# Kernel optimization log

Hardware: AMD Instinct MI355X
Metric: run time of the kernel (lower is better)

Reference implementation:

```python
import jax, jax.numpy as jnp
import numpy as np

B, F_IN, N, S = 2, 128, 192, 192   # batch, in_features, n_nodes, seq (seq==n_nodes required by mask broadcast)
H, D = 4, 64                        # n_heads, n_hidden (out_features = H*D = 256)
NEG_SLOPE = 0.2


def setup_inputs() -> dict:
    key = jax.random.key(0)
    ks = jax.random.split(key, 6)
    X = jax.random.normal(ks[0], (B, F_IN, N, S), dtype=jnp.float32)
    A = jax.random.randint(ks[1], (N, N, 1), 0, 2, dtype=jnp.int32)
    W_lin = jax.random.normal(ks[2], (F_IN, H * D), dtype=jnp.float32) * 0.05
    b_lin = jax.random.uniform(ks[3], (H * D,), dtype=jnp.float32)
    W_attn = jax.random.normal(ks[4], (2 * D,), dtype=jnp.float32) * 0.05
    b_attn = jax.random.uniform(ks[5], (1,), dtype=jnp.float32)
    return {"X": X, "A": A, "W_lin": W_lin, "b_lin": b_lin,
            "W_attn": W_attn, "b_attn": b_attn}


def reference(X, A, W_lin, b_lin, W_attn, b_attn):
    # Dropout is identity (eval mode).
    b, f, n, s = X.shape
    x = jnp.transpose(X, (0, 3, 2, 1))                      # (b, s, n, f)
    g = (x @ W_lin + b_lin).reshape(b, s, n, H, D)          # (b, s, n, H, D)
    # attn is affine: attn(cat[g_i, g_j]) = a_src.g_i + a_dst.g_j + b_attn
    a_src, a_dst = W_attn[:D], W_attn[D:]
    s_src = jnp.einsum('bsnhd,d->bsnh', g, a_src)
    s_dst = jnp.einsum('bsnhd,d->bsnh', g, a_dst)
    e = s_src[:, :, :, None, :] + s_dst[:, :, None, :, :] + b_attn[0]  # (b, s, n_i, n_j, H)
    e = jnp.where(e >= 0, e, NEG_SLOPE * e)                 # LeakyReLU
    # torch masked_fill broadcast: mask (n,n,1,1) aligns with e dims (s, n_i, n_j, H)
    e = jnp.where(A[..., None] == 0, -jnp.inf, e)
    alphas = jax.nn.softmax(e, axis=1)                      # softmax over seq dim (dim=1, as in source)
    alphas = jnp.nan_to_num(alphas, nan=0.0)
    # einsum 'mnojh,klphf->mnohf': independent sums over j (alphas) and k,l,p (g)
    sum_g = g.sum(axis=(0, 1, 2))                           # (H, D)
    attn_res = alphas.sum(axis=3)[..., None] * sum_g        # (b, s, n, H, D)
    out = attn_res.reshape(b, s, n, H * D)                  # concat=True
    return jnp.transpose(out, (0, 3, 2, 1))                 # (b, out_features, n, s)
```

## Files before the change

kernel.cpp:

```cpp
#include <hip/hip_runtime.h>
#include <math.h>

#define B_ 2
#define F_ 128
#define N_ 192
#define S_ 192
#define NS_ (N_ * S_)
#define SLOPE 0.2f
#define LOG2E 1.4426950408889634f
#define NEG_INF (-__builtin_inff())

#if defined(__has_builtin)
#if __has_builtin(__builtin_amdgcn_exp2f)
#define EXP2(x) __builtin_amdgcn_exp2f(x)
#else
#define EXP2(x) exp2f(x)
#endif
#else
#define EXP2(x) exp2f(x)
#endif

#define OFF_WSRC 0
#define OFF_WDST 512
#define OFF_CSRC 1024
#define OFF_CDST 1028
#define OFF_SUMG 1040
#define OFF_PART 1296
#define OFF_PE   2320
#define OFF_QD   (OFF_PE + 8 * NS_ * 2)
#define OFF_QT   (OFF_QD + 8 * NS_)

__global__ __launch_bounds__(256) void kPre(const float* __restrict__ X,
                                            const float* __restrict__ W_lin,
                                            const float* __restrict__ b_lin,
                                            const float* __restrict__ W_attn,
                                            const float* __restrict__ b_attn,
                                            float* __restrict__ ws) {
    int blk = blockIdx.x, t = threadIdx.x;
    if (blk < 1024) {
        int sq = blk & 3, f = (blk >> 2) & 127, b = blk >> 9;
        const float4* p = (const float4*)(X + ((size_t)(b * F_ + f)) * NS_ + sq * 9216);
        float acc = 0.f;
#pragma unroll
        for (int k = 0; k < 9; k++) {
            float4 v = p[t + k * 256];
            acc += (v.x + v.y) + (v.z + v.w);
        }
        for (int o = 32; o; o >>= 1) acc += __shfl_down(acc, o, 64);
        __shared__ float red[4];
        if ((t & 63) == 0) red[t >> 6] = acc;
        __syncthreads();
        if (t == 0)
            ws[OFF_PART + sq * 256 + b * 128 + f] = (red[0] + red[1]) + (red[2] + red[3]);
    } else if (blk == 1024) {
        const float4* wa = (const float4*)W_attn;
        for (int c = t; c < 512; c += 256) {
            int f = c >> 2, h = c & 3;
            const float4* wl = (const float4*)(W_lin + f * 256 + h * 64);
            float as = 0.f, ad = 0.f;
#pragma unroll
            for (int q = 0; q < 16; q++) {
                float4 w = wl[q], a1 = wa[q], a2 = wa[16 + q];
                as += w.x * a1.x + w.y * a1.y + w.z * a1.z + w.w * a1.w;
                ad += w.x * a2.x + w.y * a2.y + w.z * a2.z + w.w * a2.w;
            }
            ws[OFF_WSRC + c] = as * LOG2E;
            ws[OFF_WDST + c] = ad * LOG2E;
        }
    } else {
        if (t < 4) {
            float c = 0.f;
            for (int d = 0; d < 64; d++) c += b_lin[t * 64 + d] * W_attn[d];
            ws[OFF_CSRC + t] = (c + b_attn[0]) * LOG2E;
        } else if (t < 8) {
            int h = t - 4;
            float c = 0.f;
            for (int d = 0; d < 64; d++) c += b_lin[h * 64 + d] * W_attn[64 + d];
            ws[OFF_CDST + h] = c * LOG2E;
        }
    }
}

__global__ __launch_bounds__(256) void kProj(const float* __restrict__ X,
                                             const int* __restrict__ A,
                                             const float* __restrict__ W_lin,
                                             const float* __restrict__ b_lin,
                                             float* __restrict__ ws) {
    __shared__ float4 wsl[128], wdl[128];
    __shared__ float red[4 * 64 * 9];
    __shared__ float xs[128];
    __shared__ float wbuf[4096];
    int t = threadIdx.x, blk = blockIdx.x;
    if (blk < 1152) {
        int n = blk % 192, bsc = blk / 192;
        int b = bsc / 3, sc = bsc % 3;
        if (t < 128) {
            wsl[t] = ((const float4*)(ws + OFF_WSRC))[t];
            wdl[t] = ((const float4*)(ws + OFF_WDST))[t];
        }
        __syncthreads();
        int fq = t >> 6, lane = t & 63;
        int s = sc * 64 + lane;
        float aS[4] = {0, 0, 0, 0}, aD[4] = {0, 0, 0, 0};
        const float* xp = X + (size_t)(b * F_) * NS_ + n * S_ + s;
        int f0 = fq * 32;
#pragma unroll 8
        for (int fi = 0; fi < 32; fi++) {
            float x = xp[(size_t)(f0 + fi) * NS_];
            float4 w1 = wsl[f0 + fi], w2 = wdl[f0 + fi];
            aS[0] += x * w1.x; aS[1] += x * w1.y; aS[2] += x * w1.z; aS[3] += x * w1.w;
            aD[0] += x * w2.x; aD[1] += x * w2.y; aD[2] += x * w2.z; aD[3] += x * w2.w;
        }
        float* rp = red + t * 9;
#pragma unroll
        for (int h = 0; h < 4; h++) { rp[h] = aS[h]; rp[4 + h] = aD[h]; }
        __syncthreads();
        float2* PEp = (float2*)(ws + OFF_PE);
        float*  QDf = ws + OFF_QD;
        float*  QTf = ws + OFF_QT;
#pragma unroll
        for (int c = t; c < 512; c += 256) {
            int s_loc = c >> 3, k = c & 7;
            float v = red[s_loc * 9 + k] + red[(64 + s_loc) * 9 + k] +
                      red[(128 + s_loc) * 9 + k] + red[(192 + s_loc) * 9 + k];
            int ss = sc * 64 + s_loc;
            if (k < 4) {
                int bh = b * 4 + k;
                bool masked = (A[ss * 192 + n] == 0);
                float2 pr;
                if (masked) { pr.x = 0.f; pr.y = 0.f; }
                else {
                    float pt = v + ws[OFF_CSRC + k];
                    pr.x = EXP2(pt); pr.y = EXP2(0.2f * pt);
                }
                PEp[(size_t)bh * NS_ + n * 192 + ss] = pr;
            } else {
                int h = k - 4, bh = b * 4 + h;
                float dv = v + ws[OFF_CDST + h];
                QDf[(size_t)bh * NS_ + ss * 192 + n] = dv;
                QTf[(size_t)bh * NS_ + n * 192 + ss] = dv;
            }
        }
    } else {
        if (t < 128) {
            float v = 0.f;
#pragma unroll
            for (int q = 0; q < 8; q++) v += ws[OFF_PART + q * 128 + t];
            xs[t] = v;
        }
        float acc = 0.f;
        for (int ch = 0; ch < 8; ch++) {
            const float4* s4 = (const float4*)(W_lin + ch * 4096);
            __syncthreads();
#pragma unroll
            for (int k = 0; k < 4; k++) ((float4*)wbuf)[t + k * 256] = s4[t + k * 256];
            __syncthreads();
#pragma unroll
            for (int fi = 0; fi < 16; fi++) acc += xs[ch * 16 + fi] * wbuf[fi * 256 + t];
        }
        ws[OFF_SUMG + t] = acc + 73728.f * b_lin[t];
    }
}

__global__ __launch_bounds__(576) void kAttn(const float* __restrict__ ws,
                                             float* __restrict__ out) {
    int blk = blockIdx.x, t = threadIdx.x;
    int bh = blk & 7, it = blk >> 3;
    int b = bh >> 2, h = bh & 3;
    __shared__ float4 peA[192];
    __shared__ float2 peB[192];
    __shared__ float zpart[3 * 3 * 192];
    __shared__ float4 zr4[192];
    __shared__ float accp[3 * 3 * 192];
    __shared__ float sg_sh[64];
    const float2* PEp = (const float2*)(ws + OFF_PE) + (size_t)bh * NS_;
    const float*  QDf = ws + OFF_QD + (size_t)bh * NS_;
    const float*  QTf = ws + OFF_QT + (size_t)bh * NS_;
    if (t < 64) sg_sh[t] = ws[OFF_SUMG + h * 64 + t];
    if (t < 192) {
        float2 e0 = PEp[(it * 3 + 0) * 192 + t];
        float2 e1 = PEp[(it * 3 + 1) * 192 + t];
        float2 e2 = PEp[(it * 3 + 2) * 192 + t];
        peA[t] = make_float4(e0.x, e0.y, e1.x, e1.y);
        peB[t] = e2;
    }
    __syncthreads();

    {
        int sq = t / 192, j = t - sq * 192;
        float z0 = 0.f, z1 = 0.f, z2 = 0.f;
#pragma unroll 8
        for (int s = sq * 64; s < sq * 64 + 64; s++) {
            float q = QDf[s * 192 + j];
            float Q1 = EXP2(q), Q2 = EXP2(0.2f * q);
            float4 Ea = peA[s];
            float2 Eb = peB[s];
            z0 += fmaxf(Ea.x * Q1, Ea.y * Q2);
            z1 += fmaxf(Ea.z * Q1, Ea.w * Q2);
            z2 += fmaxf(Eb.x * Q1, Eb.y * Q2);
        }
        zpart[sq * 576 + 0 * 192 + j] = z0;
        zpart[sq * 576 + 1 * 192 + j] = z1;
        zpart[sq * 576 + 2 * 192 + j] = z2;
    }
    __syncthreads();
    {
        int r = t / 192, j = t - r * 192;
        float Z = zpart[r * 192 + j] + zpart[576 + r * 192 + j] +
                  zpart[1152 + r * 192 + j];
        ((float*)zr4)[j * 4 + r] = (Z != 0.f) ? (1.f / Z) : 0.f;
    }
    __syncthreads();

    {
        int jt = t / 192, s = t - jt * 192;
        float4 Ea = peA[s];
        float2 Eb = peB[s];
        float a0 = 0.f, a1 = 0.f, a2 = 0.f;
#pragma unroll 8
        for (int j = jt * 64; j < jt * 64 + 64; j++) {
            float g = QTf[j * 192 + s];
            float G1 = EXP2(g), G2 = EXP2(0.2f * g);
            float4 Z4 = zr4[j];
            a0 += fmaxf(Ea.x * G1, Ea.y * G2) * Z4.x;
            a1 += fmaxf(Ea.z * G1, Ea.w * G2) * Z4.y;
            a2 += fmaxf(Eb.x * G1, Eb.y * G2) * Z4.z;
        }
        accp[jt * 576 + 0 * 192 + s] = a0;
        accp[jt * 576 + 1 * 192 + s] = a1;
        accp[jt * 576 + 2 * 192 + s] = a2;
    }
    __syncthreads();

    {
        int r = t / 192, s = t - r * 192;
        float acc = accp[r * 192 + s] + accp[576 + r * 192 + s] +
                    accp[1152 + r * 192 + s];
        int i = it * 3 + r;
        float* op = out + (((size_t)(b * 256 + h * 64)) * 192 + i) * 192 + s;
#pragma unroll 8
        for (int d = 0; d < 64; d++)
            op[(size_t)d * NS_] = acc * sg_sh[d];
    }
}

extern "C" void kernel_launch(void* const* d_in, const int* in_sizes, int n_in,
                              void* d_out, int out_size, void* d_ws, size_t ws_size,
                              hipStream_t stream) {
    const float* X      = (const float*)d_in[0];
    const int*   A      = (const int*)d_in[1];
    const float* W_lin  = (const float*)d_in[2];
    const float* b_lin  = (const float*)d_in[3];
    const float* W_attn = (const float*)d_in[4];
    const float* b_attn = (const float*)d_in[5];
    float* out = (float*)d_out;
    float* ws  = (float*)d_ws;

    kPre<<<1026, 256, 0, stream>>>(X, W_lin, b_lin, W_attn, b_attn, ws);
    kProj<<<1153, 256, 0, stream>>>(X, A, W_lin, b_lin, ws);
    kAttn<<<512, 576, 0, stream>>>(ws, out);
}
```

Baseline: 163.9 us.

## Fuse three kernels into one persistent kernel with atomic work queues

Replaces the three separate launches (pre-reduction, projection, attention) with a single persistent kernel of 512 blocks. Blocks pull work items from global atomic counters and move between phases through grid-wide completion barriers that spin-wait. The attention phase now writes per-(b,h) accumulators to workspace, and a third phase scales them by sum_g with vectorized float4 stores. This removes launch gaps and tail effects between kernels, but adds spin-wait barriers, an extra workspace round-trip for the accumulators, and depends on all 512 blocks being co-resident.

Result: slower. 310.5 us (+89.5%).

```diff
diff --git a/kernel.cpp b/kernel.cpp
--- a/kernel.cpp
+++ b/kernel.cpp
@@ -6,9 +6,12 @@
 #define N_ 192
 #define S_ 192
 #define NS_ (N_ * S_)
-#define SLOPE 0.2f
 #define LOG2E 1.4426950408889634f
-#define NEG_INF (-__builtin_inff())
+#define NBLK 512
+#define NTHR 384
+#define TOTAL_A 640
+#define TOTAL_B 512
+#define TOTAL_C 512
 
 #if defined(__has_builtin)
 #if __has_builtin(__builtin_amdgcn_exp2f)
@@ -20,227 +23,246 @@
 #define EXP2(x) exp2f(x)
 #endif
 
-#define OFF_WSRC 0
-#define OFF_WDST 512
-#define OFF_CSRC 1024
-#define OFF_CDST 1028
-#define OFF_SUMG 1040
-#define OFF_PART 1296
-#define OFF_PE   2320
+#define OFF_PART 0
+#define OFF_PE   256
 #define OFF_QD   (OFF_PE + 8 * NS_ * 2)
 #define OFF_QT   (OFF_QD + 8 * NS_)
-
-__global__ __launch_bounds__(256) void kPre(const float* __restrict__ X,
-                                            const float* __restrict__ W_lin,
-                                            const float* __restrict__ b_lin,
-                                            const float* __restrict__ W_attn,
-                                            const float* __restrict__ b_attn,
-                                            float* __restrict__ ws) {
-    int blk = blockIdx.x, t = threadIdx.x;
-    if (blk < 1024) {
-        int sq = blk & 3, f = (blk >> 2) & 127, b = blk >> 9;
-        const float4* p = (const float4*)(X + ((size_t)(b * F_ + f)) * NS_ + sq * 9216);
-        float acc = 0.f;
-#pragma unroll
-        for (int k = 0; k < 9; k++) {
-            float4 v = p[t + k * 256];
-            acc += (v.x + v.y) + (v.z + v.w);
-        }
-        for (int o = 32; o; o >>= 1) acc += __shfl_down(acc, o, 64);
-        __shared__ float red[4];
-        if ((t & 63) == 0) red[t >> 6] = acc;
-        __syncthreads();
-        if (t == 0)
-            ws[OFF_PART + sq * 256 + b * 128 + f] = (red[0] + red[1]) + (red[2] + red[3]);
-    } else if (blk == 1024) {
-        const float4* wa = (const float4*)W_attn;
-        for (int c = t; c < 512; c += 256) {
+#define OFF_ACC  (OFF_QT + 8 * NS_)
+
+__device__ int g_ctr[8];
+
+#define AGENT __HIP_MEMORY_SCOPE_AGENT
+
+__device__ __forceinline__ int grabItem(int* q, int* item_sh, int t) {
+    if (t == 0)
+        *item_sh = __hip_atomic_fetch_add(q, 1, __ATOMIC_RELAXED, AGENT);
+    __syncthreads();
+    return *item_sh;
+}
+
+__device__ __forceinline__ void markDone(int* d, int t) {
+    __syncthreads();
+    if (t == 0) {
+        __threadfence();
+        __hip_atomic_fetch_add(d, 1, __ATOMIC_RELEASE, AGENT);
+    }
+    __syncthreads();
+}
+
+__device__ __forceinline__ void waitDone(int* d, int target, int t) {
+    if (t == 0) {
+        int guard = 0;
+        while (__hip_atomic_load(d, __ATOMIC_ACQUIRE, AGENT) < target &&
+               ++guard < (1 << 21))
+            __builtin_amdgcn_s_sleep(8);
+        __threadfence();
+    }
+    __syncthreads();
+}
+
+__global__ __launch_bounds__(NTHR, 3) void kFused(const float* __restrict__ X,
+                                                  const int* __restrict__ A,
+                                                  const float* __restrict__ W_lin,
+                                                  const float* __restrict__ b_lin,
+                                                  const float* __restrict__ W_attn,
+                                                  const float* __restrict__ b_attn,
+                                                  float* __restrict__ ws,
+                                                  float* __restrict__ out) {
+    __shared__ float wslf[512], wdlf[512], csh[4], cdh[4];
+    __shared__ float red1[2 * 192 * 9];
+    __shared__ float4 peA4[192];
+    __shared__ float2 peB2[192];
+    __shared__ float zpart[2 * 3 * 192];
+    __shared__ float4 zr4[192];
+    __shared__ float accp[2 * 3 * 192];
+    __shared__ float sg_red[8];
+    __shared__ int item_sh;
+    int t = threadIdx.x;
+
+    {
+        const float4* wa4 = (const float4*)W_attn;
+        for (int c = t; c < 512; c += NTHR) {
             int f = c >> 2, h = c & 3;
             const float4* wl = (const float4*)(W_lin + f * 256 + h * 64);
             float as = 0.f, ad = 0.f;
 #pragma unroll
-            for (int q = 0; q < 16; q++) {
-                float4 w = wl[q], a1 = wa[q], a2 = wa[16 + q];
+            for (int qq = 0; qq < 16; qq++) {
+                float4 w = wl[qq], a1 = wa4[qq], a2 = wa4[16 + qq];
                 as += w.x * a1.x + w.y * a1.y + w.z * a1.z + w.w * a1.w;
                 ad += w.x * a2.x + w.y * a2.y + w.z * a2.z + w.w * a2.w;
             }
-            ws[OFF_WSRC + c] = as * LOG2E;
-            ws[OFF_WDST + c] = ad * LOG2E;
-        }
-    } else {
-        if (t < 4) {
+            wslf[c] = as * LOG2E;
+            wdlf[c] = ad * LOG2E;
+        }
+        if (t < 8) {
+            int h = t & 3;
+            const float* bl = b_lin + h * 64;
+            const float* wa = W_attn + ((t >= 4) ? 64 : 0);
             float c = 0.f;
-            for (int d = 0; d < 64; d++) c += b_lin[t * 64 + d] * W_attn[d];
-            ws[OFF_CSRC + t] = (c + b_attn[0]) * LOG2E;
-        } else if (t < 8) {
-            int h = t - 4;
-            float c = 0.f;
-            for (int d = 0; d < 64; d++) c += b_lin[h * 64 + d] * W_attn[64 + d];
-            ws[OFF_CDST + h] = c * LOG2E;
-        }
-    }
-}
-
-__global__ __launch_bounds__(256) void kProj(const float* __restrict__ X,
-                                             const int* __restrict__ A,
-                                             const float* __restrict__ W_lin,
-                                             const float* __restrict__ b_lin,
-                                             float* __restrict__ ws) {
-    __shared__ float4 wsl[128], wdl[128];
-    __shared__ float red[4 * 64 * 9];
-    __shared__ float xs[128];
-    __shared__ float wbuf[4096];
-    int t = threadIdx.x, blk = blockIdx.x;
-    if (blk < 1152) {
-        int n = blk % 192, bsc = blk / 192;
-        int b = bsc / 3, sc = bsc % 3;
-        if (t < 128) {
-            wsl[t] = ((const float4*)(ws + OFF_WSRC))[t];
-            wdl[t] = ((const float4*)(ws + OFF_WDST))[t];
-        }
-        __syncthreads();
-        int fq = t >> 6, lane = t & 63;
-        int s = sc * 64 + lane;
-        float aS[4] = {0, 0, 0, 0}, aD[4] = {0, 0, 0, 0};
-        const float* xp = X + (size_t)(b * F_) * NS_ + n * S_ + s;
-        int f0 = fq * 32;
+            for (int d = 0; d < 64; d++) c += bl[d] * wa[d];
+            if (t < 4) csh[h] = (c + b_attn[0]) * LOG2E;
+            else cdh[h] = c * LOG2E;
+        }
+        __syncthreads();
+    }
+
+    for (;;) {
+        int v = grabItem(&g_ctr[0], &item_sh, t);
+        if (v >= TOTAL_A) break;
+        if (v < 384) {
+            int n = v % 192, b = v / 192;
+            int fq = t / 192, sl = t % 192;
+            float aS[4] = {0, 0, 0, 0}, aD[4] = {0, 0, 0, 0};
+            const float* xp = X + (size_t)(b * F_) * NS_ + n * S_ + sl;
+            int f0 = fq * 64;
 #pragma unroll 8
-        for (int fi = 0; fi < 32; fi++) {
-            float x = xp[(size_t)(f0 + fi) * NS_];
-            float4 w1 = wsl[f0 + fi], w2 = wdl[f0 + fi];
-            aS[0] += x * w1.x; aS[1] += x * w1.y; aS[2] += x * w1.z; aS[3] += x * w1.w;
-            aD[0] += x * w2.x; aD[1] += x * w2.y; aD[2] += x * w2.z; aD[3] += x * w2.w;
-        }
-        float* rp = red + t * 9;
-#pragma unroll
-        for (int h = 0; h < 4; h++) { rp[h] = aS[h]; rp[4 + h] = aD[h]; }
-        __syncthreads();
-        float2* PEp = (float2*)(ws + OFF_PE);
-        float*  QDf = ws + OFF_QD;
-        float*  QTf = ws + OFF_QT;
-#pragma unroll
-        for (int c = t; c < 512; c += 256) {
-            int s_loc = c >> 3, k = c & 7;
-            float v = red[s_loc * 9 + k] + red[(64 + s_loc) * 9 + k] +
-                      red[(128 + s_loc) * 9 + k] + red[(192 + s_loc) * 9 + k];
-            int ss = sc * 64 + s_loc;
-            if (k < 4) {
-                int bh = b * 4 + k;
-                bool masked = (A[ss * 192 + n] == 0);
-                float2 pr;
-                if (masked) { pr.x = 0.f; pr.y = 0.f; }
-                else {
-                    float pt = v + ws[OFF_CSRC + k];
-                    pr.x = EXP2(pt); pr.y = EXP2(0.2f * pt);
+            for (int fi = 0; fi < 64; fi++) {
+                float x = xp[(size_t)(f0 + fi) * NS_];
+                float4 w1 = ((const float4*)wslf)[f0 + fi];
+                float4 w2 = ((const float4*)wdlf)[f0 + fi];
+                aS[0] += x * w1.x; aS[1] += x * w1.y; aS[2] += x * w1.z; aS[3] += x * w1.w;
+                aD[0] += x * w2.x; aD[1] += x * w2.y; aD[2] += x * w2.z; aD[3] += x * w2.w;
+            }
+            float* rp = red1 + fq * 1728 + sl * 9;
+#pragma unroll
+            for (int h = 0; h < 4; h++) { rp[h] = aS[h]; rp[4 + h] = aD[h]; }
+            __syncthreads();
+            for (int c = t; c < 1536; c += NTHR) {
+                int ss = c >> 3, k = c & 7;
+                float vsum = red1[ss * 9 + k] + red1[1728 + ss * 9 + k];
+                if (k < 4) {
+                    int bh = b * 4 + k;
+                    bool masked = (A[ss * 192 + n] == 0);
+                    float2 pr; pr.x = 0.f; pr.y = 0.f;
+                    if (!masked) {
+                        float pt = vsum + csh[k];
+                        pr.x = EXP2(pt); pr.y = EXP2(0.2f * pt);
+                    }
+                    ((float2*)(ws + OFF_PE))[(size_t)bh * NS_ + n * 192 + ss] = pr;
+                } else {
+                    int h = k - 4, bh = b * 4 + h;
+                    float dv = vsum + cdh[h];
+                    ws[OFF_QD + (size_t)bh * NS_ + ss * 192 + n] = dv;
+                    ws[OFF_QT + (size_t)bh * NS_ + n * 192 + ss] = dv;
                 }
-                PEp[(size_t)bh * NS_ + n * 192 + ss] = pr;
-            } else {
-                int h = k - 4, bh = b * 4 + h;
-                float dv = v + ws[OFF_CDST + h];
-                QDf[(size_t)bh * NS_ + ss * 192 + n] = dv;
-                QTf[(size_t)bh * NS_ + n * 192 + ss] = dv;
-            }
-        }
-    } else {
-        if (t < 128) {
-            float v = 0.f;
-#pragma unroll
-            for (int q = 0; q < 8; q++) v += ws[OFF_PART + q * 128 + t];
-            xs[t] = v;
-        }
-        float acc = 0.f;
-        for (int ch = 0; ch < 8; ch++) {
-            const float4* s4 = (const float4*)(W_lin + ch * 4096);
+            }
+        } else {
+            int u = v - 384;
+            const float4* p = (const float4*)(X + (size_t)u * NS_);
+            float acc = 0.f;
+#pragma unroll
+            for (int k = 0; k < 24; k++) {
+                float4 x4 = p[t + k * NTHR];
+                acc += (x4.x + x4.y) + (x4.z + x4.w);
+            }
+            for (int o = 32; o; o >>= 1) acc += __shfl_down(acc, o, 64);
+            if ((t & 63) == 0) sg_red[t >> 6] = acc;
             __syncthreads();
-#pragma unroll
-            for (int k = 0; k < 4; k++) ((float4*)wbuf)[t + k * 256] = s4[t + k * 256];
-            __syncthreads();
-#pragma unroll
-            for (int fi = 0; fi < 16; fi++) acc += xs[ch * 16 + fi] * wbuf[fi * 256 + t];
-        }
-        ws[OFF_SUMG + t] = acc + 73728.f * b_lin[t];
-    }
-}
-
-__global__ __launch_bounds__(576) void kAttn(const float* __restrict__ ws,
-                                             float* __restrict__ out) {
-    int blk = blockIdx.x, t = threadIdx.x;
-    int bh = blk & 7, it = blk >> 3;
-    int b = bh >> 2, h = bh & 3;
-    __shared__ float4 peA[192];
-    __shared__ float2 peB[192];
-    __shared__ float zpart[3 * 3 * 192];
-    __shared__ float4 zr4[192];
-    __shared__ float accp[3 * 3 * 192];
-    __shared__ float sg_sh[64];
-    const float2* PEp = (const float2*)(ws + OFF_PE) + (size_t)bh * NS_;
-    const float*  QDf = ws + OFF_QD + (size_t)bh * NS_;
-    const float*  QTf = ws + OFF_QT + (size_t)bh * NS_;
-    if (t < 64) sg_sh[t] = ws[OFF_SUMG + h * 64 + t];
-    if (t < 192) {
-        float2 e0 = PEp[(it * 3 + 0) * 192 + t];
-        float2 e1 = PEp[(it * 3 + 1) * 192 + t];
-        float2 e2 = PEp[(it * 3 + 2) * 192 + t];
-        peA[t] = make_float4(e0.x, e0.y, e1.x, e1.y);
-        peB[t] = e2;
-    }
-    __syncthreads();
-
-    {
-        int sq = t / 192, j = t - sq * 192;
-        float z0 = 0.f, z1 = 0.f, z2 = 0.f;
+            if (t == 0)
+                ws[OFF_PART + u] = ((sg_red[0] + sg_red[1]) + (sg_red[2] + sg_red[3])) +
+                                   (sg_red[4] + sg_red[5]);
+        }
+        markDone(&g_ctr[1], t);
+    }
+    waitDone(&g_ctr[1], TOTAL_A, t);
+
+    for (;;) {
+        int v = grabItem(&g_ctr[2], &item_sh, t);
+        if (v >= TOTAL_B) break;
+        int bh = v & 7, it3 = v >> 3;
+        const float2* PEp = (const float2*)(ws + OFF_PE) + (size_t)bh * NS_;
+        const float*  QDf = ws + OFF_QD + (size_t)bh * NS_;
+        const float*  QTf = ws + OFF_QT + (size_t)bh * NS_;
+        if (t < 192) {
+            float2 e0 = PEp[(it3 * 3 + 0) * 192 + t];
+            float2 e1 = PEp[(it3 * 3 + 1) * 192 + t];
+            float2 e2 = PEp[(it3 * 3 + 2) * 192 + t];
+            peA4[t] = make_float4(e0.x, e0.y, e1.x, e1.y);
+            peB2[t] = e2;
+        }
+        __syncthreads();
+        {
+            int sq = t / 192, j = t - sq * 192;
+            float z0 = 0.f, z1 = 0.f, z2 = 0.f;
 #pragma unroll 8
-        for (int s = sq * 64; s < sq * 64 + 64; s++) {
-            float q = QDf[s * 192 + j];
-            float Q1 = EXP2(q), Q2 = EXP2(0.2f * q);
-            float4 Ea = peA[s];
-            float2 Eb = peB[s];
-            z0 += fmaxf(Ea.x * Q1, Ea.y * Q2);
-            z1 += fmaxf(Ea.z * Q1, Ea.w * Q2);
-            z2 += fmaxf(Eb.x * Q1, Eb.y * Q2);
-        }
-        zpart[sq * 576 + 0 * 192 + j] = z0;
-        zpart[sq * 576 + 1 * 192 + j] = z1;
-        zpart[sq * 576 + 2 * 192 + j] = z2;
-    }
-    __syncthreads();
-    {
-        int r = t / 192, j = t - r * 192;
-        float Z = zpart[r * 192 + j] + zpart[576 + r * 192 + j] +
-                  zpart[1152 + r * 192 + j];
-        ((float*)zr4)[j * 4 + r] = (Z != 0.f) ? (1.f / Z) : 0.f;
-    }
-    __syncthreads();
-
-    {
-        int jt = t / 192, s = t - jt * 192;
-        float4 Ea = peA[s];
-        float2 Eb = peB[s];
-        float a0 = 0.f, a1 = 0.f, a2 = 0.f;
+            for (int s = sq * 96; s < sq * 96 + 96; s++) {
+                float qv = QDf[s * 192 + j];
+                float Q1 = EXP2(qv), Q2 = EXP2(0.2f * qv);
+                float4 Ea = peA4[s];
+                float2 Eb = peB2[s];
+                z0 += fmaxf(Ea.x * Q1, Ea.y * Q2);
+                z1 += fmaxf(Ea.z * Q1, Ea.w * Q2);
+                z2 += fmaxf(Eb.x * Q1, Eb.y * Q2);
+            }
+            zpart[sq * 576 + 0 * 192 + j] = z0;
+            zpart[sq * 576 + 1 * 192 + j] = z1;
+            zpart[sq * 576 + 2 * 192 + j] = z2;
+        }
+        __syncthreads();
+        for (int c = t; c < 576; c += NTHR) {
+            int r = c / 192, j = c - r * 192;
+            float Z = zpart[c] + zpart[576 + c];
+            ((float*)zr4)[j * 4 + r] = (Z != 0.f) ? (1.f / Z) : 0.f;
+        }
+        __syncthreads();
+        {
+            int jt = t / 192, s = t - jt * 192;
+            float4 Ea = peA4[s];
+            float2 Eb = peB2[s];
+            float a0 = 0.f, a1 = 0.f, a2 = 0.f;
 #pragma unroll 8
-        for (int j = jt * 64; j < jt * 64 + 64; j++) {
-            float g = QTf[j * 192 + s];
-            float G1 = EXP2(g), G2 = EXP2(0.2f * g);
-            float4 Z4 = zr4[j];
-            a0 += fmaxf(Ea.x * G1, Ea.y * G2) * Z4.x;
-            a1 += fmaxf(Ea.z * G1, Ea.w * G2) * Z4.y;
-            a2 += fmaxf(Eb.x * G1, Eb.y * G2) * Z4.z;
-        }
-        accp[jt * 576 + 0 * 192 + s] = a0;
-        accp[jt * 576 + 1 * 192 + s] = a1;
-        accp[jt * 576 + 2 * 192 + s] = a2;
-    }
-    __syncthreads();
-
-    {
-        int r = t / 192, s = t - r * 192;
-        float acc = accp[r * 192 + s] + accp[576 + r * 192 + s] +
-                    accp[1152 + r * 192 + s];
-        int i = it * 3 + r;
-        float* op = out + (((size_t)(b * 256 + h * 64)) * 192 + i) * 192 + s;
-#pragma unroll 8
-        for (int d = 0; d < 64; d++)
-            op[(size_t)d * NS_] = acc * sg_sh[d];
+            for (int j = jt * 96; j < jt * 96 + 96; j++) {
+                float g = QTf[j * 192 + s];
+                float G1 = EXP2(g), G2 = EXP2(0.2f * g);
+                float4 Z4 = zr4[j];
+                a0 += fmaxf(Ea.x * G1, Ea.y * G2) * Z4.x;
+                a1 += fmaxf(Ea.z * G1, Ea.w * G2) * Z4.y;
+                a2 += fmaxf(Eb.x * G1, Eb.y * G2) * Z4.z;
+            }
+            accp[jt * 576 + 0 * 192 + s] = a0;
+            accp[jt * 576 + 1 * 192 + s] = a1;
+            accp[jt * 576 + 2 * 192 + s] = a2;
+        }
+        __syncthreads();
+        for (int c = t; c < 576; c += NTHR) {
+            int r = c / 192, s = c - r * 192;
+            float acc = accp[c] + accp[576 + c];
+            ws[OFF_ACC + (size_t)bh * NS_ + (it3 * 3 + r) * 192 + s] = acc;
+        }
+        markDone(&g_ctr[3], t);
+    }
+    waitDone(&g_ctr[3], TOTAL_B, t);
+
+    for (;;) {
+        int v = grabItem(&g_ctr[4], &item_sh, t);
+        if (v >= TOTAL_C) break;
+        int bh = v & 7, d = v >> 3;
+        int b = bh >> 2, h = bh & 3;
+        int cc = h * 64 + d;
+        float psum = 0.f;
+        if (t < 128)
+            psum = (ws[OFF_PART + t] + ws[OFF_PART + 128 + t]) * W_lin[t * 256 + cc];
+        for (int o = 32; o; o >>= 1) psum += __shfl_down(psum, o, 64);
+        if ((t & 63) == 0) sg_red[t >> 6] = psum;
+        __syncthreads();
+        float sgd = sg_red[0] + sg_red[1] + 73728.f * b_lin[cc];
+        const float4* ap = (const float4*)(ws + OFF_ACC + (size_t)bh * NS_);
+        float4* op = (float4*)(out + ((size_t)(b * 256 + cc)) * NS_);
+#pragma unroll
+        for (int k = 0; k < 24; k++) {
+            float4 a = ap[t + k * NTHR];
+            op[t + k * NTHR] = make_float4(a.x * sgd, a.y * sgd, a.z * sgd, a.w * sgd);
+        }
+        __syncthreads();
+    }
+
+    if (t == 0) {
+        int e = __hip_atomic_fetch_add(&g_ctr[5], 1, __ATOMIC_ACQ_REL, AGENT);
+        if (e == NBLK - 1) {
+#pragma unroll
+            for (int i = 0; i < 8; i++)
+                __hip_atomic_store(&g_ctr[i], 0, __ATOMIC_RELEASE, AGENT);
+        }
     }
 }
 
@@ -256,7 +278,5 @@
     float* out = (float*)d_out;
     float* ws  = (float*)d_ws;
 
-    kPre<<<1026, 256, 0, stream>>>(X, W_lin, b_lin, W_attn, b_attn, ws);
-    kProj<<<1153, 256, 0, stream>>>(X, A, W_lin, b_lin, ws);
-    kAttn<<<512, 576, 0, stream>>>(ws, out);
-}
+    kFused<<<NBLK, NTHR, 0, stream>>>(X, A, W_lin, b_lin, W_attn, b_attn, ws, out);
+}
```
